# Performance work log

Measured on AMD Instinct MI355X. Metric: run time of the kernel, lower is better.

## Reference

```python
import jax, jax.numpy as jnp
import numpy as np

L, B, T, D, H, FF = 4, 8, 1024, 256, 8, 1024
DK = D // H
SCALE = 1.0 / np.sqrt(DK)


def _ln(x, g, b, eps=1e-6):
    m = jnp.mean(x, axis=-1, keepdims=True)
    v = jnp.mean(jnp.square(x - m), axis=-1, keepdims=True)
    return (x - m) * jax.lax.rsqrt(v + eps) * g + b


def _l2norm(x, eps=1e-8):
    n = jnp.sqrt(jnp.sum(jnp.square(x), axis=-1, keepdims=True))
    return x / jnp.maximum(n, eps)


def setup_inputs() -> dict:
    key = jax.random.key(0)
    ks = jax.random.split(key, 8)
    s = 0.02
    inp = {
        'x': jax.random.normal(ks[0], (B, T, D), dtype=jnp.float32),
        'padding_mask': jnp.zeros((B, T), dtype=bool),
        'ln1_g': jnp.ones((L, D), jnp.float32), 'ln1_b': jnp.zeros((L, D), jnp.float32),
        'qn_g': jnp.ones((L, D), jnp.float32), 'qn_b': jnp.zeros((L, D), jnp.float32),
        'Wqkv': jax.random.normal(ks[1], (L, 3 * D, D), jnp.float32) * s,
        'bqkv': jnp.zeros((L, 3 * D), jnp.float32),
        'Wo': jax.random.normal(ks[2], (L, D, D), jnp.float32) * s,
        'bo': jnp.zeros((L, D), jnp.float32),
        'ln2_g': jnp.ones((L, D), jnp.float32), 'ln2_b': jnp.zeros((L, D), jnp.float32),
        'W1': jax.random.normal(ks[3], (L, FF, D), jnp.float32) * s,
        'b1': jnp.zeros((L, FF), jnp.float32),
        'W2': jax.random.normal(ks[4], (L, D, FF), jnp.float32) * s,
        'b2': jnp.zeros((L, D), jnp.float32),
        'alpha': jnp.full((L,), 0.1, jnp.float32),
        'beta': jnp.full((L,), 0.1, jnp.float32),
    }
    return inp


def _block(x, pad_mask, p):
    (g1, bb1, qg, qb, wqkv, bqkv, wo, bo, g2, bb2, w1, b1, w2, b2, a, be) = p
    Bn, Tn, Dn = x.shape
    # --- SemiCausalAttention on norm1(x) ---
    xn = _ln(x, g1, bb1)
    h = _ln(xn, qg, qb)                      # q_norm LayerNorm
    qkv = h @ wqkv.T + bqkv                  # [B,T,3D]
    qkv = qkv.reshape(Bn, Tn, 3, H, DK).transpose(2, 0, 3, 1, 4)  # [3,B,H,T,dk]
    Q, K, V = qkv[0], qkv[1], qkv[2]
    Q = _l2norm(Q)
    K = _l2norm(K)
    scores = jnp.einsum('bhtd,bhsd->bhts', Q, K) * SCALE
    scores = jnp.clip(scores, -10.0, 10.0)
    causal = jnp.triu(jnp.ones((Tn, Tn), dtype=bool), k=1)        # True = future
    scores = jnp.where(causal[None, None], -10000.0, scores)
    scores = jnp.where(pad_mask[:, None, None, :], -10000.0, scores)
    attn = jax.nn.softmax(scores, axis=-1)
    ao = jnp.einsum('bhts,bhsd->bhtd', attn, V)                   # [B,H,T,dk]
    ao = ao.transpose(0, 2, 1, 3).reshape(Bn, Tn, Dn)
    attn_out = (ao @ wo.T + bo) * 0.5
    x = x + jnp.tanh(a) * attn_out
    # --- FFN ---
    f = _ln(x, g2, bb2)
    f = jax.nn.gelu(f @ w1.T + b1, approximate=False)
    f = f @ w2.T + b2
    x = x + jnp.tanh(be) * f
    return jnp.clip(x, -100.0, 100.0)


def reference(x, padding_mask, ln1_g, ln1_b, qn_g, qn_b, Wqkv, bqkv, Wo, bo,
              ln2_g, ln2_b, W1, b1, W2, b2, alpha, beta):
    params = (ln1_g, ln1_b, qn_g, qn_b, Wqkv, bqkv, Wo, bo,
              ln2_g, ln2_b, W1, b1, W2, b2, alpha, beta)

    def step(carry, p):
        return _block(carry, padding_mask, p), None

    out, _ = jax.lax.scan(step, x, params)
    return out
```

## Files before the change

### kernel.cpp

```cpp
#include <hip/hip_runtime.h>
#include <hip/hip_bf16.h>
#include <math.h>

#define BB 8
#define TT 1024
#define DD 256
#define HH 8
#define BT 8192

typedef __attribute__((ext_vector_type(4))) float f32x4;
typedef __attribute__((ext_vector_type(16))) float f32x16;
typedef __attribute__((ext_vector_type(8))) short short8;
typedef __attribute__((ext_vector_type(4))) short short4v;
typedef __attribute__((ext_vector_type(8))) __bf16 bf16x8;

__device__ inline float bf2f(short s) {
  unsigned int u = ((unsigned int)(unsigned short)s) << 16;
  return __builtin_bit_cast(float, u);
}
__device__ inline short f2bf(float f) {
  unsigned int u = __builtin_bit_cast(unsigned int, f);
  unsigned int lsb = (u >> 16) & 1u;
  u += 0x7fffu + lsb;
  return (short)(u >> 16);
}
__device__ inline unsigned int cvtpk(float lo, float hi) {
  unsigned int r;
  asm("v_cvt_pk_bf16_f32 %0, %1, %2" : "=v"(r) : "v"(lo), "v"(hi));
  return r;
}

__device__ inline f32x4 mfma16(short8 a, short8 b, f32x4 c) {
  return __builtin_amdgcn_mfma_f32_16x16x32_bf16(
      __builtin_bit_cast(bf16x8, a), __builtin_bit_cast(bf16x8, b), c, 0, 0, 0);
}
__device__ inline f32x16 mfma32(short8 a, short8 b, f32x16 c) {
  return __builtin_amdgcn_mfma_f32_32x32x16_bf16(
      __builtin_bit_cast(bf16x8, a), __builtin_bit_cast(bf16x8, b), c, 0, 0, 0);
}

__device__ inline void gload_lds16(void* lds, const void* g) {
  __builtin_amdgcn_global_load_lds(
      (const __attribute__((address_space(1))) unsigned int*)g,
      (__attribute__((address_space(3))) unsigned int*)lds, 16, 0, 0);
}

__global__ void cvt_kernel(const float4* __restrict__ src, short4v* __restrict__ dst, int n4) {
  int i = blockIdx.x * 256 + threadIdx.x;
  if (i < n4) {
    float4 v = src[i];
    short4v o;
    o[0] = f2bf(v.x); o[1] = f2bf(v.y); o[2] = f2bf(v.z); o[3] = f2bf(v.w);
    dst[i] = o;
  }
}

__global__ __launch_bounds__(256) void ln_kernel(
    const float* __restrict__ Xin,
    const float* __restrict__ g1, const float* __restrict__ b1,
    const float* __restrict__ g2, const float* __restrict__ b2,
    short* __restrict__ out, int dbl)
{
  const int row = blockIdx.x * 4 + (threadIdx.x >> 6);
  const int lane = threadIdx.x & 63;
  const float4 v = *(const float4*)(Xin + (size_t)row * 256 + lane * 4);
  float y[4] = {v.x, v.y, v.z, v.w};

  float s = y[0] + y[1] + y[2] + y[3];
  #pragma unroll
  for (int m = 32; m >= 1; m >>= 1) s += __shfl_xor(s, m, 64);
  float mean = s * (1.0f / 256.0f);
  float sq = 0.f;
  #pragma unroll
  for (int i = 0; i < 4; ++i) { y[i] -= mean; sq += y[i] * y[i]; }
  #pragma unroll
  for (int m = 32; m >= 1; m >>= 1) sq += __shfl_xor(sq, m, 64);
  float rs = rsqrtf(sq * (1.0f / 256.0f) + 1e-6f);
  #pragma unroll
  for (int i = 0; i < 4; ++i) y[i] = y[i] * rs * g1[lane * 4 + i] + b1[lane * 4 + i];

  if (dbl) {
    float s2 = y[0] + y[1] + y[2] + y[3];
    #pragma unroll
    for (int m = 32; m >= 1; m >>= 1) s2 += __shfl_xor(s2, m, 64);
    float m2 = s2 * (1.0f / 256.0f);
    float sq2 = 0.f;
    #pragma unroll
    for (int i = 0; i < 4; ++i) { y[i] -= m2; sq2 += y[i] * y[i]; }
    #pragma unroll
    for (int m = 32; m >= 1; m >>= 1) sq2 += __shfl_xor(sq2, m, 64);
    float rs2 = rsqrtf(sq2 * (1.0f / 256.0f) + 1e-6f);
    #pragma unroll
    for (int i = 0; i < 4; ++i) y[i] = y[i] * rs2 * g2[lane * 4 + i] + b2[lane * 4 + i];
  }
  #pragma unroll
  for (int i = 0; i < 4; ++i) out[(size_t)row * 256 + lane * 4 + i] = f2bf(y[i]);
}

__global__ __launch_bounds__(256) void qknorm_kernel(short* __restrict__ qkv) {
  const int row = blockIdx.x * 4 + (threadIdx.x >> 6);
  const int lane = threadIdx.x & 63;
  short* p = qkv + (size_t)row * 768 + lane * 8;
  short8 v = *(short8*)p;
  float f[8]; float ss = 0.f;
  #pragma unroll
  for (int j = 0; j < 8; ++j) { f[j] = bf2f(v[j]); ss += f[j] * f[j]; }
  ss += __shfl_xor(ss, 1, 64);
  ss += __shfl_xor(ss, 2, 64);
  float inv = 1.0f / fmaxf(sqrtf(ss), 1e-8f);
  const float C2 = 0.25503489702966368f;
  float sc = (lane < 32) ? inv * C2 : inv;
  short8 o;
  #pragma unroll
  for (int j = 0; j < 8; ++j) o[j] = f2bf(f[j] * sc);
  *(short8*)p = o;
}

template<int BN, int EPI>
__global__ __launch_bounds__(256) void gemm_bt(
    const short* __restrict__ A, const short* __restrict__ Bw,
    const float* __restrict__ bias, float* __restrict__ X,
    short* __restrict__ Obf, const float* __restrict__ scale_p,
    int M, int N, int K)
{
  constexpr int MI = (BN == 128) ? 4 : 2;
  __shared__ __align__(16) short A_s[128 * 64];
  __shared__ __align__(16) short B_s[BN * 64];
  const int tid = threadIdx.x;
  const int lane = tid & 63;
  const int w = tid >> 6;
  const int lo4 = lane & 15, hi2 = lane >> 4;
  int wm, wn0;
  if (BN == 128) { wm = (w >> 1) * 64; wn0 = (w & 1) * 64; }
  else           { wm = w * 32;        wn0 = 0; }
  const int bid = blockIdx.x + blockIdx.y * gridDim.x;
  const int nwg = gridDim.x * gridDim.y;
  const int wg = (bid & 7) * (nwg >> 3) + (bid >> 3);
  const int tM = (wg / gridDim.x) * 128, tN = (wg % gridDim.x) * BN;

  f32x4 acc[MI][4];
  #pragma unroll
  for (int i = 0; i < MI; ++i)
    #pragma unroll
    for (int j = 0; j < 4; ++j) acc[i][j] = (f32x4){0.f, 0.f, 0.f, 0.f};

  const int swz = (lo4 & 7) << 3;

  for (int k0 = 0; k0 < K; k0 += 64) {
    #pragma unroll
    for (int ri = 0; ri < 4; ++ri) {
      int o = ri * 2048 + tid * 8;
      int row = o >> 6;
      int col = (o & 63) ^ ((row & 7) << 3);
      gload_lds16(&A_s[ri * 2048 + w * 512], A + (size_t)(tM + row) * K + k0 + col);
    }
    #pragma unroll
    for (int ri = 0; ri < BN / 32; ++ri) {
      int o = ri * 2048 + tid * 8;
      int row = o >> 6;
      int col = (o & 63) ^ ((row & 7) << 3);
      gload_lds16(&B_s[ri * 2048 + w * 512], Bw + (size_t)(tN + row) * K + k0 + col);
    }
    __syncthreads();
    #pragma unroll
    for (int kc = 0; kc < 2; ++kc) {
      short8 af[MI], bfr[4];
      #pragma unroll
      for (int i = 0; i < MI; ++i)
        af[i] = *(const short8*)&A_s[(wm + i * 16 + lo4) * 64 + ((kc * 32 + hi2 * 8) ^ swz)];
      #pragma unroll
      for (int j = 0; j < 4; ++j)
        bfr[j] = *(const short8*)&B_s[(wn0 + j * 16 + lo4) * 64 + ((kc * 32 + hi2 * 8) ^ swz)];
      #pragma unroll
      for (int i = 0; i < MI; ++i)
        #pragma unroll
        for (int j = 0; j < 4; ++j)
          acc[i][j] = mfma16(af[i], bfr[j], acc[i][j]);
    }
    __syncthreads();
  }

  float ts = 0.f;
  if (EPI == 1 || EPI == 3) ts = tanhf(scale_p[0]);

  #pragma unroll
  for (int i = 0; i < MI; ++i) {
    #pragma unroll
    for (int j = 0; j < 4; ++j) {
      #pragma unroll
      for (int r = 0; r < 4; ++r) {
        int row = tM + wm + i * 16 + hi2 * 4 + r;
        int col = tN + wn0 + j * 16 + lo4;
        float v = acc[i][j][r] + bias[col];
        size_t idx = (size_t)row * N + col;
        if (EPI == 0) {
          Obf[idx] = f2bf(v);
        } else if (EPI == 1) {
          X[idx] += ts * (v * 0.5f);
        } else if (EPI == 2) {
          float gl = 0.5f * v * (1.0f + erff(v * 0.70710678118f));
          Obf[idx] = f2bf(gl);
        } else {
          float o = X[idx] + ts * v;
          o = fminf(100.f, fmaxf(-100.f, o));
          X[idx] = o;
        }
      }
    }
  }
}

template<int EPI>
__global__ __launch_bounds__(256) void gemm64(
    const short* __restrict__ A, const short* __restrict__ Bw,
    const float* __restrict__ bias, float* __restrict__ X,
    const float* __restrict__ scale_p, int M, int N, int K)
{
  __shared__ __align__(16) short A_s[64 * 64];
  __shared__ __align__(16) short B_s[64 * 64];
  const int tid = threadIdx.x;
  const int lane = tid & 63;
  const int w = tid >> 6;
  const int lo4 = lane & 15, hi2 = lane >> 4;
  const int wm = (w >> 1) * 32, wn0 = (w & 1) * 32;
  const int bid = blockIdx.x + blockIdx.y * gridDim.x;
  const int nwg = gridDim.x * gridDim.y;
  const int wg = (bid & 7) * (nwg >> 3) + (bid >> 3);
  const int tM = (wg / gridDim.x) * 64, tN = (wg % gridDim.x) * 64;

  f32x4 acc[2][2];
  #pragma unroll
  for (int i = 0; i < 2; ++i)
    #pragma unroll
    for (int j = 0; j < 2; ++j) acc[i][j] = (f32x4){0.f, 0.f, 0.f, 0.f};

  const int swz = (lo4 & 7) << 3;

  for (int k0 = 0; k0 < K; k0 += 64) {
    #pragma unroll
    for (int ri = 0; ri < 2; ++ri) {
      int o = ri * 2048 + tid * 8;
      int row = o >> 6;
      int col = (o & 63) ^ ((row & 7) << 3);
      gload_lds16(&A_s[ri * 2048 + w * 512], A + (size_t)(tM + row) * K + k0 + col);
      gload_lds16(&B_s[ri * 2048 + w * 512], Bw + (size_t)(tN + row) * K + k0 + col);
    }
    __syncthreads();
    #pragma unroll
    for (int kc = 0; kc < 2; ++kc) {
      short8 af[2], bfr[2];
      #pragma unroll
      for (int i = 0; i < 2; ++i)
        af[i] = *(const short8*)&A_s[(wm + i * 16 + lo4) * 64 + ((kc * 32 + hi2 * 8) ^ swz)];
      #pragma unroll
      for (int j = 0; j < 2; ++j)
        bfr[j] = *(const short8*)&B_s[(wn0 + j * 16 + lo4) * 64 + ((kc * 32 + hi2 * 8) ^ swz)];
      #pragma unroll
      for (int i = 0; i < 2; ++i)
        #pragma unroll
        for (int j = 0; j < 2; ++j)
          acc[i][j] = mfma16(af[i], bfr[j], acc[i][j]);
    }
    __syncthreads();
  }

  float ts = tanhf(scale_p[0]);

  #pragma unroll
  for (int i = 0; i < 2; ++i) {
    #pragma unroll
    for (int j = 0; j < 2; ++j) {
      #pragma unroll
      for (int r = 0; r < 4; ++r) {
        int row = tM + wm + i * 16 + hi2 * 4 + r;
        int col = tN + wn0 + j * 16 + lo4;
        float v = acc[i][j][r] + bias[col];
        size_t idx = (size_t)row * N + col;
        if (EPI == 1) {
          X[idx] += ts * (v * 0.5f);
        } else {
          float o = X[idx] + ts * v;
          o = fminf(100.f, fmaxf(-100.f, o));
          X[idx] = o;
        }
      }
    }
  }
}

#define KG_BODY_G(KG, PKO, MASKED)                                                 \
  {                                                                                \
    const short* kp = Kbase + (size_t)(t * 64 + (KG) * 32 + lo5) * 768;            \
    short8 kf0 = *(const short8*)(kp + hi1 * 8);                                   \
    short8 kf1 = *(const short8*)(kp + 16 + hi1 * 8);                              \
    f32x16 z = (f32x16)0.0f;                                                       \
    z = mfma32(kf0, qb[0], z);                                                     \
    z = mfma32(kf1, qb[1], z);                                                     \
    float pr[16];                                                                  \
    _Pragma("unroll")                                                              \
    for (int r = 0; r < 16; ++r) {                                                 \
      float sv = __builtin_amdgcn_fmed3f(z[r], -14.4269504f, 14.4269504f);         \
      float pe;                                                                    \
      asm("v_exp_f32 %0, %1" : "=v"(pe) : "v"(sv));                                \
      const int keyrel = (r & 3) + 8 * (r >> 2) + 4 * hi1;                         \
      if (MASKED) pe = (keyrel > lo5) ? 0.f : pe;                                  \
      if (pm) pe = ((pm >> ((KG) * 32 + keyrel)) & 1ull) ? 0.f : pe;               \
      pr[r] = pe;                                                                  \
      rsum += pe;                                                                  \
    }                                                                              \
    _Pragma("unroll")                                                              \
    for (int i = 0; i < 8; ++i) PKO[i] = cvtpk(pr[2 * i], pr[2 * i + 1]);          \
  }

#define PV_CHUNK_G(K2, PKO)                                                        \
  {                                                                                \
    const int half = (K2) & 1;                                                     \
    unsigned int keep0 = hi1 ? PKO[4 * half + 2] : PKO[4 * half + 0];              \
    unsigned int keep1 = hi1 ? PKO[4 * half + 3] : PKO[4 * half + 1];              \
    unsigned int send0 = hi1 ? PKO[4 * half + 0] : PKO[4 * half + 2];              \
    unsigned int send1 = hi1 ? PKO[4 * half + 1] : PKO[4 * half + 3];              \
    unsigned int r0 = (unsigned int)__shfl_xor((int)send0, 32, 64);                \
    unsigned int r1 = (unsigned int)__shfl_xor((int)send1, 32, 64);                \
    union { unsigned int u[4]; short8 s; } fa;                                     \
    fa.u[0] = hi1 ? r0 : keep0;                                                    \
    fa.u[1] = hi1 ? r1 : keep1;                                                    \
    fa.u[2] = hi1 ? keep0 : r0;                                                    \
    fa.u[3] = hi1 ? keep1 : r1;                                                    \
    short8 vb;                                                                     \
    _Pragma("unroll")                                                              \
    for (int jj = 0; jj < 8; ++jj)                                                 \
      vb[jj] = Vbase[(size_t)(t * 64 + (K2) * 16 + hi1 * 8 + jj) * 768 + lo5];     \
    if ((K2) & 1) oaccB = mfma32(fa.s, vb, oaccB);                                 \
    else          oaccA = mfma32(fa.s, vb, oaccA);                                 \
  }

__global__ __launch_bounds__(256) void attn_kernel(
    const short* __restrict__ qkv, const unsigned char* __restrict__ pad,
    short* __restrict__ ao)
{
  const int tid = threadIdx.x, lane = tid & 63, w = tid >> 6;
  const int lo5 = lane & 31, hi1 = lane >> 5;
  const int bid = blockIdx.x;
  const int b = bid & 7;
  const int h = (bid >> 3) & 7;
  const int bj = bid >> 6;
  const int j = w * 8 + bj;
  const size_t rowbase = (size_t)b * TT;
  const int qrow = j * 32 + lo5;
  const int ntile = (j >> 1) + 1;

  const short* Kbase = qkv + rowbase * 768 + 256 + h * 32;
  const short* Vbase = qkv + rowbase * 768 + 512 + h * 32;

  short8 qb[2];
  #pragma unroll
  for (int c2 = 0; c2 < 2; ++c2)
    qb[c2] = *(const short8*)(qkv + (rowbase + qrow) * 768 + h * 32 + c2 * 16 + hi1 * 8);

  f32x16 oaccA = (f32x16)0.0f;
  f32x16 oaccB = (f32x16)0.0f;
  float rsum = 0.f;

  int t = 0;
  #pragma unroll 2
  for (; t < ntile - 1; ++t) {
    const unsigned long long pm = __ballot(pad[rowbase + t * 64 + lane] != 0);
    unsigned int pk0[8], pk1[8];
    KG_BODY_G(0, pk0, false)
    PV_CHUNK_G(0, pk0)
    PV_CHUNK_G(1, pk0)
    KG_BODY_G(1, pk1, false)
    PV_CHUNK_G(2, pk1)
    PV_CHUNK_G(3, pk1)
  }
  {
    const unsigned long long pm = __ballot(pad[rowbase + t * 64 + lane] != 0);
    unsigned int pk0[8], pk1[8];
    if (j & 1) {
      KG_BODY_G(0, pk0, false)
      PV_CHUNK_G(0, pk0)
      PV_CHUNK_G(1, pk0)
      KG_BODY_G(1, pk1, true)
      PV_CHUNK_G(2, pk1)
      PV_CHUNK_G(3, pk1)
    } else {
      KG_BODY_G(0, pk0, true)
      PV_CHUNK_G(0, pk0)
      PV_CHUNK_G(1, pk0)
    }
  }

  rsum += __shfl_xor(rsum, 32, 64);
  float rinv = 1.0f / fmaxf(rsum, 1e-30f);
  #pragma unroll
  for (int r = 0; r < 16; ++r) {
    int ql = (r & 3) + 8 * (r >> 2) + 4 * hi1;
    float riv = __shfl(rinv, ql, 64);
    int qg = j * 32 + ql;
    ao[(rowbase + qg) * 256 + h * 32 + lo5] = f2bf((oaccA[r] + oaccB[r]) * riv);
  }
}

extern "C" void kernel_launch(void* const* d_in, const int* in_sizes, int n_in,
                              void* d_out, int out_size, void* d_ws, size_t ws_size,
                              hipStream_t stream) {
  const float* x_in  = (const float*)d_in[0];
  const unsigned char* pad = (const unsigned char*)d_in[1];
  const float* ln1_g = (const float*)d_in[2];
  const float* ln1_b = (const float*)d_in[3];
  const float* qn_g  = (const float*)d_in[4];
  const float* qn_b  = (const float*)d_in[5];
  const float* Wqkv  = (const float*)d_in[6];
  const float* bqkv  = (const float*)d_in[7];
  const float* Wo    = (const float*)d_in[8];
  const float* bo    = (const float*)d_in[9];
  const float* ln2_g = (const float*)d_in[10];
  const float* ln2_b = (const float*)d_in[11];
  const float* W1    = (const float*)d_in[12];
  const float* b1    = (const float*)d_in[13];
  const float* W2    = (const float*)d_in[14];
  const float* b2    = (const float*)d_in[15];
  const float* alpha = (const float*)d_in[16];
  const float* beta  = (const float*)d_in[17];

  char* ws = (char*)d_ws;
  size_t off = 0;
  short* wqkv_bf = (short*)(ws + off); off += (size_t)4 * 768 * 256 * 2;
  short* wo_bf   = (short*)(ws + off); off += (size_t)4 * 256 * 256 * 2;
  short* w1_bf   = (short*)(ws + off); off += (size_t)4 * 1024 * 256 * 2;
  short* w2_bf   = (short*)(ws + off); off += (size_t)4 * 256 * 1024 * 2;
  short* h_bf    = (short*)(ws + off); off += (size_t)BT * 256 * 2;
  short* qkv_bf  = (short*)(ws + off); off += (size_t)BT * 768 * 2;
  short* ao_bf   = (short*)(ws + off); off += (size_t)BT * 256 * 2;
  short* g_bf    = (short*)(ws + off); off += (size_t)BT * 1024 * 2;

  float* X = (float*)d_out;

  hipMemcpyAsync(d_out, x_in, (size_t)BT * DD * 4, hipMemcpyDeviceToDevice, stream);
  cvt_kernel<<<768,  256, 0, stream>>>((const float4*)Wqkv, (short4v*)wqkv_bf, 4 * 768 * 256 / 4);
  cvt_kernel<<<256,  256, 0, stream>>>((const float4*)Wo,   (short4v*)wo_bf,   4 * 256 * 256 / 4);
  cvt_kernel<<<1024, 256, 0, stream>>>((const float4*)W1,   (short4v*)w1_bf,   4 * 1024 * 256 / 4);
  cvt_kernel<<<1024, 256, 0, stream>>>((const float4*)W2,   (short4v*)w2_bf,   4 * 256 * 1024 / 4);

  for (int l = 0; l < 4; ++l) {
    ln_kernel<<<2048, 256, 0, stream>>>(X, ln1_g + l * 256, ln1_b + l * 256,
                                        qn_g + l * 256, qn_b + l * 256, h_bf, 1);
    gemm_bt<128, 0><<<dim3(6, 64), 256, 0, stream>>>(h_bf, wqkv_bf + (size_t)l * 768 * 256,
                                                     bqkv + l * 768, nullptr, qkv_bf, nullptr,
                                                     8192, 768, 256);
    qknorm_kernel<<<2048, 256, 0, stream>>>(qkv_bf);
    attn_kernel<<<512, 256, 0, stream>>>(qkv_bf, pad, ao_bf);
    gemm64<1><<<dim3(4, 128), 256, 0, stream>>>(ao_bf, wo_bf + (size_t)l * 256 * 256,
                                                bo + l * 256, X, alpha + l,
                                                8192, 256, 256);
    ln_kernel<<<2048, 256, 0, stream>>>(X, ln2_g + l * 256, ln2_b + l * 256,
                                        nullptr, nullptr, h_bf, 0);
    gemm_bt<128, 2><<<dim3(8, 64), 256, 0, stream>>>(h_bf, w1_bf + (size_t)l * 1024 * 256,
                                                     b1 + l * 1024, nullptr, g_bf, nullptr,
                                                     8192, 1024, 256);
    gemm64<3><<<dim3(4, 128), 256, 0, stream>>>(g_bf, w2_bf + (size_t)l * 256 * 1024,
                                                b2 + l * 256, X, beta + l,
                                                8192, 256, 1024);
  }
}
```

Measured before the change: 376.1 us.

## Fuse QK l2norm into QKV GEMM epilogue, split attention KV across warps

The per-head L2 normalization of Q and K moves into the QKV GEMM epilogue, using cross-lane shuffles over each 32-wide head. This removes the separate qknorm pass that re-read and re-wrote the QKV buffer. The attention kernel now pairs causal query tiles (j and 31-j) per block to balance work, and splits each tile's key range between two warps that reduce through shared memory. That doubles the grid to 1024 blocks for more parallelism, at the cost of an extra sync and LDS reduction. The four weight-conversion launches are also merged into one kernel.

Result: slower. 462.9 us (+23.1%).

```diff
diff --git a/kernel.cpp b/kernel.cpp
--- a/kernel.cpp
+++ b/kernel.cpp
@@ -45,14 +45,23 @@
       (__attribute__((address_space(3))) unsigned int*)lds, 16, 0, 0);
 }
 
-__global__ void cvt_kernel(const float4* __restrict__ src, short4v* __restrict__ dst, int n4) {
+__global__ __launch_bounds__(256) void cvt_all(
+    const float4* __restrict__ s0, short4v* __restrict__ d0, int n0,
+    const float4* __restrict__ s1, short4v* __restrict__ d1, int n1,
+    const float4* __restrict__ s2, short4v* __restrict__ d2, int n2,
+    const float4* __restrict__ s3, short4v* __restrict__ d3, int n3)
+{
   int i = blockIdx.x * 256 + threadIdx.x;
-  if (i < n4) {
-    float4 v = src[i];
-    short4v o;
-    o[0] = f2bf(v.x); o[1] = f2bf(v.y); o[2] = f2bf(v.z); o[3] = f2bf(v.w);
-    dst[i] = o;
-  }
+  const float4* s; short4v* d;
+  if (i < n0) { s = s0 + i; d = d0 + i; }
+  else if ((i -= n0) < n1) { s = s1 + i; d = d1 + i; }
+  else if ((i -= n1) < n2) { s = s2 + i; d = d2 + i; }
+  else if ((i -= n2) < n3) { s = s3 + i; d = d3 + i; }
+  else return;
+  float4 v = *s;
+  short4v o;
+  o[0] = f2bf(v.x); o[1] = f2bf(v.y); o[2] = f2bf(v.z); o[3] = f2bf(v.w);
+  *d = o;
 }
 
 __global__ __launch_bounds__(256) void ln_kernel(
@@ -95,25 +104,6 @@
   }
   #pragma unroll
   for (int i = 0; i < 4; ++i) out[(size_t)row * 256 + lane * 4 + i] = f2bf(y[i]);
-}
-
-__global__ __launch_bounds__(256) void qknorm_kernel(short* __restrict__ qkv) {
-  const int row = blockIdx.x * 4 + (threadIdx.x >> 6);
-  const int lane = threadIdx.x & 63;
-  short* p = qkv + (size_t)row * 768 + lane * 8;
-  short8 v = *(short8*)p;
-  float f[8]; float ss = 0.f;
-  #pragma unroll
-  for (int j = 0; j < 8; ++j) { f[j] = bf2f(v[j]); ss += f[j] * f[j]; }
-  ss += __shfl_xor(ss, 1, 64);
-  ss += __shfl_xor(ss, 2, 64);
-  float inv = 1.0f / fmaxf(sqrtf(ss), 1e-8f);
-  const float C2 = 0.25503489702966368f;
-  float sc = (lane < 32) ? inv * C2 : inv;
-  short8 o;
-  #pragma unroll
-  for (int j = 0; j < 8; ++j) o[j] = f2bf(f[j] * sc);
-  *(short8*)p = o;
 }
 
 template<int BN, int EPI>
@@ -180,8 +170,47 @@
     __syncthreads();
   }
 
-  float ts = 0.f;
-  if (EPI == 1 || EPI == 3) ts = tanhf(scale_p[0]);
+  if (EPI == 4) {
+    #pragma unroll
+    for (int i = 0; i < MI; ++i)
+      #pragma unroll
+      for (int j = 0; j < 4; ++j)
+        #pragma unroll
+        for (int r = 0; r < 4; ++r)
+          acc[i][j][r] += bias[tN + wn0 + j * 16 + lo4];
+    if (tN < 512) {
+      const float C2 = 0.25503489702966368f;
+      const float sc = (tN < 256) ? C2 : 1.0f;
+      #pragma unroll
+      for (int i = 0; i < MI; ++i) {
+        #pragma unroll
+        for (int r = 0; r < 4; ++r) {
+          float s01 = acc[i][0][r] * acc[i][0][r] + acc[i][1][r] * acc[i][1][r];
+          float s23 = acc[i][2][r] * acc[i][2][r] + acc[i][3][r] * acc[i][3][r];
+          #pragma unroll
+          for (int m = 1; m <= 8; m <<= 1) {
+            s01 += __shfl_xor(s01, m, 64);
+            s23 += __shfl_xor(s23, m, 64);
+          }
+          float n01 = sc / fmaxf(sqrtf(s01), 1e-8f);
+          float n23 = sc / fmaxf(sqrtf(s23), 1e-8f);
+          acc[i][0][r] *= n01; acc[i][1][r] *= n01;
+          acc[i][2][r] *= n23; acc[i][3][r] *= n23;
+        }
+      }
+    }
+    #pragma unroll
+    for (int i = 0; i < MI; ++i)
+      #pragma unroll
+      for (int j = 0; j < 4; ++j)
+        #pragma unroll
+        for (int r = 0; r < 4; ++r) {
+          int row = tM + wm + i * 16 + hi2 * 4 + r;
+          int col = tN + wn0 + j * 16 + lo4;
+          Obf[(size_t)row * N + col] = f2bf(acc[i][j][r]);
+        }
+    return;
+  }
 
   #pragma unroll
   for (int i = 0; i < MI; ++i) {
@@ -193,17 +222,11 @@
         int col = tN + wn0 + j * 16 + lo4;
         float v = acc[i][j][r] + bias[col];
         size_t idx = (size_t)row * N + col;
-        if (EPI == 0) {
-          Obf[idx] = f2bf(v);
-        } else if (EPI == 1) {
-          X[idx] += ts * (v * 0.5f);
-        } else if (EPI == 2) {
+        if (EPI == 2) {
           float gl = 0.5f * v * (1.0f + erff(v * 0.70710678118f));
           Obf[idx] = f2bf(gl);
         } else {
-          float o = X[idx] + ts * v;
-          o = fminf(100.f, fmaxf(-100.f, o));
-          X[idx] = o;
+          Obf[idx] = f2bf(v);
         }
       }
     }
@@ -314,11 +337,11 @@
 
 #define PV_CHUNK_G(K2, PKO)                                                        \
   {                                                                                \
-    const int half = (K2) & 1;                                                     \
-    unsigned int keep0 = hi1 ? PKO[4 * half + 2] : PKO[4 * half + 0];              \
-    unsigned int keep1 = hi1 ? PKO[4 * half + 3] : PKO[4 * half + 1];              \
-    unsigned int send0 = hi1 ? PKO[4 * half + 0] : PKO[4 * half + 2];              \
-    unsigned int send1 = hi1 ? PKO[4 * half + 1] : PKO[4 * half + 3];              \
+    const int half_ = (K2) & 1;                                                    \
+    unsigned int keep0 = hi1 ? PKO[4 * half_ + 2] : PKO[4 * half_ + 0];            \
+    unsigned int keep1 = hi1 ? PKO[4 * half_ + 3] : PKO[4 * half_ + 1];            \
+    unsigned int send0 = hi1 ? PKO[4 * half_ + 0] : PKO[4 * half_ + 2];            \
+    unsigned int send1 = hi1 ? PKO[4 * half_ + 1] : PKO[4 * half_ + 3];            \
     unsigned int r0 = (unsigned int)__shfl_xor((int)send0, 32, 64);                \
     unsigned int r1 = (unsigned int)__shfl_xor((int)send1, 32, 64);                \
     union { unsigned int u[4]; short8 s; } fa;                                     \
@@ -334,17 +357,20 @@
     else          oaccA = mfma32(fa.s, vb, oaccA);                                 \
   }
 
-__global__ __launch_bounds__(256) void attn_kernel(
+__global__ __launch_bounds__(256, 4) void attn_kernel(
     const short* __restrict__ qkv, const unsigned char* __restrict__ pad,
     short* __restrict__ ao)
 {
+  __shared__ float Red[2][17][64];
   const int tid = threadIdx.x, lane = tid & 63, w = tid >> 6;
   const int lo5 = lane & 31, hi1 = lane >> 5;
   const int bid = blockIdx.x;
   const int b = bid & 7;
   const int h = (bid >> 3) & 7;
   const int bj = bid >> 6;
-  const int j = w * 8 + bj;
+  const int p = w >> 1;
+  const int half = w & 1;
+  const int j = p ? (31 - bj) : bj;
   const size_t rowbase = (size_t)b * TT;
   const int qrow = j * 32 + lo5;
   const int ntile = (j >> 1) + 1;
@@ -361,22 +387,17 @@
   f32x16 oaccB = (f32x16)0.0f;
   float rsum = 0.f;
 
-  int t = 0;
-  #pragma unroll 2
-  for (; t < ntile - 1; ++t) {
+  for (int t = half; t < ntile; t += 2) {
     const unsigned long long pm = __ballot(pad[rowbase + t * 64 + lane] != 0);
     unsigned int pk0[8], pk1[8];
-    KG_BODY_G(0, pk0, false)
-    PV_CHUNK_G(0, pk0)
-    PV_CHUNK_G(1, pk0)
-    KG_BODY_G(1, pk1, false)
-    PV_CHUNK_G(2, pk1)
-    PV_CHUNK_G(3, pk1)
-  }
-  {
-    const unsigned long long pm = __ballot(pad[rowbase + t * 64 + lane] != 0);
-    unsigned int pk0[8], pk1[8];
-    if (j & 1) {
+    if (t + 1 < ntile) {
+      KG_BODY_G(0, pk0, false)
+      PV_CHUNK_G(0, pk0)
+      PV_CHUNK_G(1, pk0)
+      KG_BODY_G(1, pk1, false)
+      PV_CHUNK_G(2, pk1)
+      PV_CHUNK_G(3, pk1)
+    } else if (j & 1) {
       KG_BODY_G(0, pk0, false)
       PV_CHUNK_G(0, pk0)
       PV_CHUNK_G(1, pk0)
@@ -390,14 +411,25 @@
     }
   }
 
-  rsum += __shfl_xor(rsum, 32, 64);
-  float rinv = 1.0f / fmaxf(rsum, 1e-30f);
-  #pragma unroll
-  for (int r = 0; r < 16; ++r) {
-    int ql = (r & 3) + 8 * (r >> 2) + 4 * hi1;
-    float riv = __shfl(rinv, ql, 64);
-    int qg = j * 32 + ql;
-    ao[(rowbase + qg) * 256 + h * 32 + lo5] = f2bf((oaccA[r] + oaccB[r]) * riv);
+  if (half) {
+    #pragma unroll
+    for (int r = 0; r < 16; ++r) Red[p][r][lane] = oaccA[r] + oaccB[r];
+    Red[p][16][lane] = rsum;
+  }
+  __syncthreads();
+  if (!half) {
+    #pragma unroll
+    for (int r = 0; r < 16; ++r) oaccA[r] += oaccB[r] + Red[p][r][lane];
+    rsum += Red[p][16][lane];
+    rsum += __shfl_xor(rsum, 32, 64);
+    float rinv = 1.0f / fmaxf(rsum, 1e-30f);
+    #pragma unroll
+    for (int r = 0; r < 16; ++r) {
+      int ql = (r & 3) + 8 * (r >> 2) + 4 * hi1;
+      float riv = __shfl(rinv, ql, 64);
+      int qg = j * 32 + ql;
+      ao[(rowbase + qg) * 256 + h * 32 + lo5] = f2bf(oaccA[r] * riv);
+    }
   }
 }
 
@@ -437,19 +469,19 @@
   float* X = (float*)d_out;
 
   hipMemcpyAsync(d_out, x_in, (size_t)BT * DD * 4, hipMemcpyDeviceToDevice, stream);
-  cvt_kernel<<<768,  256, 0, stream>>>((const float4*)Wqkv, (short4v*)wqkv_bf, 4 * 768 * 256 / 4);
-  cvt_kernel<<<256,  256, 0, stream>>>((const float4*)Wo,   (short4v*)wo_bf,   4 * 256 * 256 / 4);
-  cvt_kernel<<<1024, 256, 0, stream>>>((const float4*)W1,   (short4v*)w1_bf,   4 * 1024 * 256 / 4);
-  cvt_kernel<<<1024, 256, 0, stream>>>((const float4*)W2,   (short4v*)w2_bf,   4 * 256 * 1024 / 4);
+  cvt_all<<<3072, 256, 0, stream>>>(
+      (const float4*)Wqkv, (short4v*)wqkv_bf, 4 * 768 * 256 / 4,
+      (const float4*)Wo,   (short4v*)wo_bf,   4 * 256 * 256 / 4,
+      (const float4*)W1,   (short4v*)w1_bf,   4 * 1024 * 256 / 4,
+      (const float4*)W2,   (short4v*)w2_bf,   4 * 256 * 1024 / 4);
 
   for (int l = 0; l < 4; ++l) {
     ln_kernel<<<2048, 256, 0, stream>>>(X, ln1_g + l * 256, ln1_b + l * 256,
                                         qn_g + l * 256, qn_b + l * 256, h_bf, 1);
-    gemm_bt<128, 0><<<dim3(6, 64), 256, 0, stream>>>(h_bf, wqkv_bf + (size_t)l * 768 * 256,
+    gemm_bt<128, 4><<<dim3(6, 64), 256, 0, stream>>>(h_bf, wqkv_bf + (size_t)l * 768 * 256,
                                                      bqkv + l * 768, nullptr, qkv_bf, nullptr,
                                                      8192, 768, 256);
-    qknorm_kernel<<<2048, 256, 0, stream>>>(qkv_bf);
-    attn_kernel<<<512, 256, 0, stream>>>(qkv_bf, pad, ao_bf);
+    attn_kernel<<<1024, 256, 0, stream>>>(qkv_bf, pad, ao_bf);
     gemm64<1><<<dim3(4, 128), 256, 0, stream>>>(ao_bf, wo_bf + (size_t)l * 256 * 256,
                                                 bo + l * 256, X, alpha + l,
                                                 8192, 256, 256);
```
